# Performance work log

Hardware: AMD Instinct MI355X
Metric: run time of the kernel (lower is better)

The kernel has to match this reference:

```python
import jax, jax.numpy as jnp
import numpy as np
from jax import lax

LIN_DIMS = [(3200, 2048), (2048, 1024), (1024, 512), (512, 256), (256, 128),
            (128, 64), (64, 32), (32, 16), (16, 8), (8, 4), (4, 2), (2, 1)]
BN_EPS = 1e-5


def _conv(x, w, b):
    y = lax.conv_general_dilated(x, w, window_strides=(3, 3),
                                 padding=((1, 1), (1, 1)),
                                 dimension_numbers=('NCHW', 'OIHW', 'NCHW'))
    return y + b.reshape(1, -1, 1, 1)


def _bn(x, g, b):
    # training-mode BatchNorm2d: biased batch statistics over (N, H, W)
    m = jnp.mean(x, axis=(0, 2, 3), keepdims=True)
    v = jnp.var(x, axis=(0, 2, 3), keepdims=True)
    return (x - m) * lax.rsqrt(v + BN_EPS) * g.reshape(1, -1, 1, 1) + b.reshape(1, -1, 1, 1)


def setup_inputs() -> dict:
    key = jax.random.key(0)
    ks = iter(jax.random.split(key, 64))
    d = {}
    d['x'] = jax.random.normal(next(ks), (64, 512, 40, 40), jnp.float32)
    d['conv1_w'] = jax.random.normal(next(ks), (256, 512, 3, 3), jnp.float32) / np.sqrt(512 * 9)
    d['conv1_b'] = jnp.zeros((256,), jnp.float32)
    d['bn1_g'] = jnp.ones((256,), jnp.float32)
    d['bn1_b'] = jnp.zeros((256,), jnp.float32)
    d['conv2_w'] = jax.random.normal(next(ks), (128, 256, 3, 3), jnp.float32) / np.sqrt(256 * 9)
    d['conv2_b'] = jnp.zeros((128,), jnp.float32)
    d['bn2_g'] = jnp.ones((128,), jnp.float32)
    d['bn2_b'] = jnp.zeros((128,), jnp.float32)
    for i, (fin, fout) in enumerate(LIN_DIMS):
        d[f'w{i+3}'] = jax.random.normal(next(ks), (fout, fin), jnp.float32) / np.sqrt(fin)
        d[f'b{i+3}'] = jax.random.normal(next(ks), (fout,), jnp.float32) * 0.01
    return d


def reference(x, conv1_w, conv1_b, bn1_g, bn1_b, conv2_w, conv2_b, bn2_g, bn2_b,
              w3, b3, w4, b4, w5, b5, w6, b6, w7, b7, w8, b8, w9, b9,
              w10, b10, w11, b11, w12, b12, w13, b13, w14, b14):
    h = _bn(_conv(x, conv1_w, conv1_b), bn1_g, bn1_b)          # [B,256,14,14]
    h = _bn(_conv(h, conv2_w, conv2_b), bn2_g, bn2_b)          # [B,128,5,5]
    h = h.reshape(h.shape[0], 3200)
    for w, b in [(w3, b3), (w4, b4), (w5, b5), (w6, b6), (w7, b7), (w8, b8),
                 (w9, b9), (w10, b10), (w11, b11), (w12, b12), (w13, b13), (w14, b14)]:
        h = h @ w.T + b
    return jax.nn.sigmoid(h)                                   # [B,1]
```

## Files before the change

### kernel.cpp

```cpp
#include <hip/hip_runtime.h>
#include <cstdint>
#include <cstddef>

typedef short bf16x8 __attribute__((ext_vector_type(8)));
typedef float f32x4 __attribute__((ext_vector_type(4)));

__device__ __forceinline__ unsigned short f2bf(float f) {
  union { float f; unsigned u; } v; v.f = f;
  unsigned r = v.u + 0x7fffu + ((v.u >> 16) & 1u);
  return (unsigned short)(r >> 16);
}

#define GLOAD_LDS16(gp, lp)                                            \
  __builtin_amdgcn_global_load_lds(                                    \
      (const __attribute__((address_space(1))) void*)(const void*)(gp),\
      (__attribute__((address_space(3))) void*)(void*)(lp), 16, 0, 0)

__global__ __launch_bounds__(256) void cast_bf16(const float* __restrict__ in,
                                                 unsigned short* __restrict__ out, int n4) {
  int i = blockIdx.x * 256 + threadIdx.x;
  if (i < n4) {
    float4 v = ((const float4*)in)[i];
    ushort4 o;
    o.x = f2bf(v.x); o.y = f2bf(v.y); o.z = f2bf(v.z); o.w = f2bf(v.w);
    ((ushort4*)out)[i] = o;
  }
}

__global__ __launch_bounds__(256) void im2col1(const float* __restrict__ x,
                                               unsigned short* __restrict__ A1) {
  __shared__ float buf[64 * 126];
  int t = threadIdx.x;
  int cc = blockIdx.x, oh = blockIdx.y, n = blockIdx.z;
  int ci0 = cc * 64;
  int ih0 = oh * 3 - 1;
  for (int rowid = t; rowid < 192; rowid += 256) {
    int c = rowid / 3, r = rowid - c * 3;
    buf[c * 126 + r * 42 + 0] = 0.f;
    buf[c * 126 + r * 42 + 41] = 0.f;
  }
  for (int idx = t; idx < 1920; idx += 256) {
    int row = idx / 10, ch = idx - row * 10;
    int c = row / 3, r = row - c * 3;
    int ih = ih0 + r;
    float4 v = make_float4(0.f, 0.f, 0.f, 0.f);
    if ((unsigned)ih < 40u)
      v = *(const float4*)(x + (((size_t)n * 512 + ci0 + c) * 40 + ih) * 40 + ch * 4);
    float* dst = buf + c * 126 + r * 42 + 1 + ch * 4;
    dst[0] = v.x; dst[1] = v.y; dst[2] = v.z; dst[3] = v.w;
  }
  __syncthreads();
  for (int idx = t; idx < 2016; idx += 256) {
    int ow = idx / 144, q4 = idx - ow * 144;
    int kk = q4 * 4;
    unsigned short vv[4];
#pragma unroll
    for (int j = 0; j < 4; ++j) {
      int k = kk + j;
      int c = k / 9, rr = k - c * 9;
      int kh = rr / 3, kw = rr - kh * 3;
      vv[j] = f2bf(buf[c * 126 + kh * 42 + 3 * ow + kw]);
    }
    ushort4 o; o.x = vv[0]; o.y = vv[1]; o.z = vv[2]; o.w = vv[3];
    *(ushort4*)(A1 + ((size_t)(n * 196 + oh * 14 + ow)) * 4608 + cc * 576 + kk) = o;
  }
}

__global__ __launch_bounds__(256) void im2col2(const float* __restrict__ C1,
                                               const float* __restrict__ scale,
                                               const float* __restrict__ shift,
                                               unsigned short* __restrict__ A2) {
  unsigned idx = blockIdx.x * 256u + threadIdx.x;
  unsigned m = idx / 2304u;
  unsigned k = idx - m * 2304u;
  unsigned n = m / 25u, sp = m - n * 25u;
  unsigned oh = sp / 5u, ow = sp - oh * 5u;
  int ci = (int)(k / 9u); int r = (int)k - ci * 9;
  int kh = r / 3, kw = r - kh * 3;
  int ih = (int)oh * 3 - 1 + kh, iw = (int)ow * 3 - 1 + kw;
  float v = 0.f;
  if ((unsigned)ih < 14u && (unsigned)iw < 14u)
    v = C1[((size_t)n * 196 + ih * 14 + iw) * 256 + ci] * scale[ci] + shift[ci];
  A2[idx] = f2bf(v);
}

template <int BN>
__global__ __launch_bounds__(256) void gemm_bf16(const unsigned short* __restrict__ A,
                                                 const unsigned short* __restrict__ B,
                                                 float* __restrict__ C,
                                                 int M, int N, int K) {
  __shared__ __align__(16) unsigned short As[64 * 32];
  __shared__ __align__(16) unsigned short Bs[BN * 32];
  constexpr int WN = BN / 2;
  constexpr int NT = WN / 16;
  int m0 = blockIdx.x * 64;
  int n0 = blockIdx.y * BN;
  int t = threadIdx.x;
  int wave = t >> 6, lane = t & 63;
  (void)wave; (void)lane;
  int q = (t & 63) >> 4, mr = t & 15;
  int wm = ((t >> 6) & 1) * 32;
  int wn = (t >> 7) * WN;
  f32x4 acc[2][NT] = {};

  for (int k0 = 0; k0 < K; k0 += 32) {
    __syncthreads();
    GLOAD_LDS16(A + (size_t)(m0 + (t >> 2)) * K + k0 + (t & 3) * 8, As + t * 8);
#pragma unroll
    for (int i = 0; i < BN / 64; ++i) {
      int c = t + i * 256;
      GLOAD_LDS16(B + (size_t)(n0 + (c >> 2)) * K + k0 + (c & 3) * 8, Bs + c * 8);
    }
    __syncthreads();
    bf16x8 af[2];
#pragma unroll
    for (int s = 0; s < 2; ++s)
      af[s] = *((const bf16x8*)(As + (wm + s * 16 + mr) * 32 + q * 8));
#pragma unroll
    for (int nt = 0; nt < NT; ++nt) {
      bf16x8 bfr = *((const bf16x8*)(Bs + (wn + nt * 16 + mr) * 32 + q * 8));
#pragma unroll
      for (int s = 0; s < 2; ++s)
        acc[s][nt] = __builtin_amdgcn_mfma_f32_16x16x32_bf16(af[s], bfr, acc[s][nt], 0, 0, 0);
    }
  }
#pragma unroll
  for (int s = 0; s < 2; ++s)
#pragma unroll
    for (int nt = 0; nt < NT; ++nt)
#pragma unroll
      for (int r = 0; r < 4; ++r)
        C[(size_t)(m0 + wm + s * 16 + q * 4 + r) * N + n0 + wn + nt * 16 + mr] = acc[s][nt][r];
}

__global__ void bn_stats(const float* __restrict__ C, float* __restrict__ sum,
                         float* __restrict__ sumsq, int rowsPerBlock, int ncols) {
  int c = threadIdx.x;
  int r0 = blockIdx.x * rowsPerBlock;
  float s = 0.f, s2 = 0.f;
  for (int r = 0; r < rowsPerBlock; ++r) {
    float v = C[(size_t)(r0 + r) * ncols + c];
    s += v; s2 += v * v;
  }
  atomicAdd(&sum[c], s);
  atomicAdd(&sumsq[c], s2);
}

__global__ void bn_scale(const float* __restrict__ sum, const float* __restrict__ sumsq,
                         const float* __restrict__ g, const float* __restrict__ b,
                         float* __restrict__ scale, float* __restrict__ shift,
                         float inv_count, int nc) {
  int c = blockIdx.x * blockDim.x + threadIdx.x;
  if (c < nc) {
    float m = sum[c] * inv_count;
    float var = sumsq[c] * inv_count - m * m;
    float sc = g[c] / sqrtf(var + 1e-5f);
    scale[c] = sc;
    shift[c] = b[c] - m * sc;
  }
}

__global__ void mlp_head(const float* w14, const float* b14,
                         const float* w13, const float* b13,
                         const float* w12, const float* b12,
                         const float* w11, const float* b11,
                         const float* w10, const float* b10,
                         const float* w9,  const float* b9,
                         const float* w8,  const float* b8,
                         const float* w7,  const float* b7,
                         float* __restrict__ r_out, float* __restrict__ c_out) {
  __shared__ float ra[256], rb[256];
  int t = threadIdx.x;
  float cs = 0.f;
  if (t < 2) ra[t] = w14[t];
  if (t == 0) cs = b14[0];
  __syncthreads();
  const float* Ws[7] = {w13, w12, w11, w10, w9, w8, w7};
  const float* Bs[7] = {b13, b12, b11, b10, b9, b8, b7};
  const int fouts[7] = {2, 4, 8, 16, 32, 64, 128};
  float* cur = ra; float* nxt = rb;
  for (int s = 0; s < 7; ++s) {
    int fo = fouts[s], fi = fo * 2;
    if (t == 0) {
      float d = 0.f;
      for (int i = 0; i < fo; ++i) d += cur[i] * Bs[s][i];
      cs += d;
    }
    if (t < fi) {
      float a = 0.f;
      const float* W = Ws[s];
      for (int i = 0; i < fo; ++i) a += cur[i] * W[i * fi + t];
      nxt[t] = a;
    }
    __syncthreads();
    float* tmp = cur; cur = nxt; nxt = tmp;
  }
  r_out[t] = cur[t];
  if (t == 0) c_out[0] = cs;
}

__global__ void mlp_stage(const float* __restrict__ W, const float* __restrict__ bt,
                          const float* __restrict__ r_in, const float* __restrict__ c_in,
                          float* __restrict__ r_out, float* __restrict__ c_out,
                          int fin, int fout) {
  __shared__ float red[256];
  int t = threadIdx.x;
  int jl = t & 31, ig = t >> 5;
  int j = blockIdx.x * 32 + jl;
  int chunk = fout >> 3;
  int i0 = ig * chunk;
  float acc = 0.f;
  for (int i = i0; i < i0 + chunk; ++i)
    acc += r_in[i] * W[(size_t)i * fin + j];
  red[t] = acc;
  __syncthreads();
  if (ig == 0) {
    float s = 0.f;
#pragma unroll
    for (int u = 0; u < 8; ++u) s += red[u * 32 + jl];
    r_out[j] = s;
  }
  if (blockIdx.x == 0) {
    __syncthreads();
    float p = 0.f;
    for (int i = t; i < fout; i += 256) p += r_in[i] * bt[i];
    red[t] = p;
    __syncthreads();
    for (int s = 128; s > 0; s >>= 1) {
      if (t < s) red[t] += red[t + s];
      __syncthreads();
    }
    if (t == 0) c_out[0] = red[0] + c_in[0];
  }
}

__global__ void final_k(const float* __restrict__ C2, const float* __restrict__ scale2,
                        const float* __restrict__ shift2, const float* __restrict__ r,
                        const float* __restrict__ c_in, float* __restrict__ out) {
  int n = blockIdx.x;
  int t = threadIdx.x;
  float acc = 0.f;
  for (int j = t; j < 3200; j += 256) {
    int c = j / 25, sp = j - c * 25;
    float v = C2[((size_t)n * 25 + sp) * 128 + c] * scale2[c] + shift2[c];
    acc += v * r[j];
  }
  __shared__ float red[256];
  red[t] = acc;
  __syncthreads();
  for (int s = 128; s > 0; s >>= 1) {
    if (t < s) red[t] += red[t + s];
    __syncthreads();
  }
  if (t == 0) {
    float z = red[0] + c_in[0];
    out[n] = 1.f / (1.f + expf(-z));
  }
}

static constexpr size_t OFF_A1   = 0;
static constexpr size_t OFF_W1B  = 115605504;
static constexpr size_t OFF_C1   = 117964800;
static constexpr size_t OFF_A2   = 130809856;
static constexpr size_t OFF_W2B  = 138182656;
static constexpr size_t OFF_C2   = 138772480;
static constexpr size_t OFF_SUM1 = 139591680;
static constexpr size_t OFF_SQ1  = 139592704;
static constexpr size_t OFF_SUM2 = 139593728;
static constexpr size_t OFF_SQ2  = 139594752;
static constexpr size_t OFF_SC1  = 139595776;
static constexpr size_t OFF_SH1  = 139596800;
static constexpr size_t OFF_SC2  = 139597824;
static constexpr size_t OFF_SH2  = 139598848;
static constexpr size_t OFF_RA   = 139599872;
static constexpr size_t OFF_RB   = 139612928;
static constexpr size_t OFF_CA   = 139625984;
static constexpr size_t OFF_CB   = 139626240;

extern "C" void kernel_launch(void* const* d_in, const int* in_sizes, int n_in,
                              void* d_out, int out_size, void* d_ws, size_t ws_size,
                              hipStream_t stream) {
  const float* x   = (const float*)d_in[0];
  const float* w1  = (const float*)d_in[1];
  const float* g1  = (const float*)d_in[3];
  const float* bb1 = (const float*)d_in[4];
  const float* w2  = (const float*)d_in[5];
  const float* g2  = (const float*)d_in[7];
  const float* bb2 = (const float*)d_in[8];

  char* ws = (char*)d_ws;
  unsigned short* A1  = (unsigned short*)(ws + OFF_A1);
  unsigned short* W1b = (unsigned short*)(ws + OFF_W1B);
  float*          C1  = (float*)(ws + OFF_C1);
  unsigned short* A2  = (unsigned short*)(ws + OFF_A2);
  unsigned short* W2b = (unsigned short*)(ws + OFF_W2B);
  float*          C2  = (float*)(ws + OFF_C2);
  float* SUM1 = (float*)(ws + OFF_SUM1);
  float* SQ1  = (float*)(ws + OFF_SQ1);
  float* SUM2 = (float*)(ws + OFF_SUM2);
  float* SQ2  = (float*)(ws + OFF_SQ2);
  float* SC1  = (float*)(ws + OFF_SC1);
  float* SH1  = (float*)(ws + OFF_SH1);
  float* SC2  = (float*)(ws + OFF_SC2);
  float* SH2  = (float*)(ws + OFF_SH2);
  float* RA   = (float*)(ws + OFF_RA);
  float* RB   = (float*)(ws + OFF_RB);
  float* CA   = (float*)(ws + OFF_CA);
  float* CB   = (float*)(ws + OFF_CB);

  hipMemsetAsync(ws + OFF_SUM1, 0, 4096, stream);

  cast_bf16<<<1152, 256, 0, stream>>>(w1, W1b, 294912);
  cast_bf16<<<288, 256, 0, stream>>>(w2, W2b, 73728);

  im2col1<<<dim3(8, 14, 64), 256, 0, stream>>>(x, A1);
  gemm_bf16<128><<<dim3(196, 2), 256, 0, stream>>>(A1, W1b, C1, 12544, 256, 4608);
  bn_stats<<<98, 256, 0, stream>>>(C1, SUM1, SQ1, 128, 256);
  bn_scale<<<1, 256, 0, stream>>>(SUM1, SQ1, g1, bb1, SC1, SH1, 1.f / 12544.f, 256);

  im2col2<<<14400, 256, 0, stream>>>(C1, SC1, SH1, A2);
  gemm_bf16<64><<<dim3(25, 2), 256, 0, stream>>>(A2, W2b, C2, 1600, 128, 2304);
  bn_stats<<<16, 128, 0, stream>>>(C2, SUM2, SQ2, 100, 128);
  bn_scale<<<1, 256, 0, stream>>>(SUM2, SQ2, g2, bb2, SC2, SH2, 1.f / 1600.f, 128);

  mlp_head<<<1, 256, 0, stream>>>(
      (const float*)d_in[31], (const float*)d_in[32],
      (const float*)d_in[29], (const float*)d_in[30],
      (const float*)d_in[27], (const float*)d_in[28],
      (const float*)d_in[25], (const float*)d_in[26],
      (const float*)d_in[23], (const float*)d_in[24],
      (const float*)d_in[21], (const float*)d_in[22],
      (const float*)d_in[19], (const float*)d_in[20],
      (const float*)d_in[17], (const float*)d_in[18],
      RA, CA);
  mlp_stage<<<16, 256, 0, stream>>>((const float*)d_in[15], (const float*)d_in[16],
                                    RA, CA, RB, CB, 512, 256);
  mlp_stage<<<32, 256, 0, stream>>>((const float*)d_in[13], (const float*)d_in[14],
                                    RB, CB, RA, CA, 1024, 512);
  mlp_stage<<<64, 256, 0, stream>>>((const float*)d_in[11], (const float*)d_in[12],
                                    RA, CA, RB, CB, 2048, 1024);
  mlp_stage<<<100, 256, 0, stream>>>((const float*)d_in[9], (const float*)d_in[10],
                                     RB, CB, RA, CA, 3200, 2048);

  final_k<<<64, 256, 0, stream>>>(C2, SC2, SH2, RA, CA, (float*)d_out);
}
```

Measured before the change: 936.2 us.

## Split-K both conv GEMMs with fused partial reduction and BN stats

Adds a blockIdx.z split-K dimension to the bf16 GEMM. Conv1 uses up to 4 K-slices, chosen by available workspace, and conv2 uses 8, to fill more CUs than the 392 and 50 block grids did. Partial sums are combined in a new reduce_stats kernel that also accumulates the BN sum and sum-of-squares. bn_scale is folded into im2col2 and final_k, and the two weight casts are merged into one launch, removing several small launches. The cost is extra global traffic to write and read the partial buffers, plus BN scale being recomputed per element. The workspace layout is reshuffled so C1 reuses A1's region.

```diff
diff --git a/kernel.cpp b/kernel.cpp
--- a/kernel.cpp
+++ b/kernel.cpp
@@ -16,15 +16,19 @@
       (const __attribute__((address_space(1))) void*)(const void*)(gp),\
       (__attribute__((address_space(3))) void*)(void*)(lp), 16, 0, 0)
 
-__global__ __launch_bounds__(256) void cast_bf16(const float* __restrict__ in,
-                                                 unsigned short* __restrict__ out, int n4) {
+__global__ __launch_bounds__(256) void cast2(const float* __restrict__ w1,
+                                             const float* __restrict__ w2,
+                                             unsigned short* __restrict__ W1b,
+                                             unsigned short* __restrict__ W2b) {
   int i = blockIdx.x * 256 + threadIdx.x;
-  if (i < n4) {
-    float4 v = ((const float4*)in)[i];
-    ushort4 o;
-    o.x = f2bf(v.x); o.y = f2bf(v.y); o.z = f2bf(v.z); o.w = f2bf(v.w);
-    ((ushort4*)out)[i] = o;
-  }
+  const float* src; unsigned short* dst; int j;
+  if (i < 294912) { src = w1; dst = W1b; j = i; }
+  else if (i < 368640) { src = w2; dst = W2b; j = i - 294912; }
+  else return;
+  float4 v = ((const float4*)src)[j];
+  ushort4 o;
+  o.x = f2bf(v.x); o.y = f2bf(v.y); o.z = f2bf(v.z); o.w = f2bf(v.w);
+  ((ushort4*)dst)[j] = o;
 }
 
 __global__ __launch_bounds__(256) void im2col1(const float* __restrict__ x,
@@ -67,8 +71,10 @@
 }
 
 __global__ __launch_bounds__(256) void im2col2(const float* __restrict__ C1,
-                                               const float* __restrict__ scale,
-                                               const float* __restrict__ shift,
+                                               const float* __restrict__ SUM1,
+                                               const float* __restrict__ SQ1,
+                                               const float* __restrict__ g,
+                                               const float* __restrict__ b,
                                                unsigned short* __restrict__ A2) {
   unsigned idx = blockIdx.x * 256u + threadIdx.x;
   unsigned m = idx / 2304u;
@@ -79,31 +85,37 @@
   int kh = r / 3, kw = r - kh * 3;
   int ih = (int)oh * 3 - 1 + kh, iw = (int)ow * 3 - 1 + kw;
   float v = 0.f;
-  if ((unsigned)ih < 14u && (unsigned)iw < 14u)
-    v = C1[((size_t)n * 196 + ih * 14 + iw) * 256 + ci] * scale[ci] + shift[ci];
+  if ((unsigned)ih < 14u && (unsigned)iw < 14u) {
+    float mean = SUM1[ci] * (1.f / 12544.f);
+    float var = SQ1[ci] * (1.f / 12544.f) - mean * mean;
+    float sc = g[ci] / sqrtf(var + 1e-5f);
+    float sh = b[ci] - mean * sc;
+    v = C1[((size_t)n * 196 + ih * 14 + iw) * 256 + ci] * sc + sh;
+  }
   A2[idx] = f2bf(v);
 }
 
 template <int BN>
 __global__ __launch_bounds__(256) void gemm_bf16(const unsigned short* __restrict__ A,
                                                  const unsigned short* __restrict__ B,
-                                                 float* __restrict__ C,
-                                                 int M, int N, int K) {
+                                                 float* __restrict__ Cp,
+                                                 int M, int N, int K, int k_chunk) {
   __shared__ __align__(16) unsigned short As[64 * 32];
   __shared__ __align__(16) unsigned short Bs[BN * 32];
   constexpr int WN = BN / 2;
   constexpr int NT = WN / 16;
   int m0 = blockIdx.x * 64;
   int n0 = blockIdx.y * BN;
-  int t = threadIdx.x;
-  int wave = t >> 6, lane = t & 63;
-  (void)wave; (void)lane;
+  int kb = blockIdx.z;
+  Cp += (size_t)kb * M * N;
+  int k_begin = kb * k_chunk;
+  int t = threadIdx.x;
   int q = (t & 63) >> 4, mr = t & 15;
   int wm = ((t >> 6) & 1) * 32;
   int wn = (t >> 7) * WN;
   f32x4 acc[2][NT] = {};
 
-  for (int k0 = 0; k0 < K; k0 += 32) {
+  for (int k0 = k_begin; k0 < k_begin + k_chunk; k0 += 32) {
     __syncthreads();
     GLOAD_LDS16(A + (size_t)(m0 + (t >> 2)) * K + k0 + (t & 3) * 8, As + t * 8);
 #pragma unroll
@@ -130,34 +142,26 @@
     for (int nt = 0; nt < NT; ++nt)
 #pragma unroll
       for (int r = 0; r < 4; ++r)
-        C[(size_t)(m0 + wm + s * 16 + q * 4 + r) * N + n0 + wn + nt * 16 + mr] = acc[s][nt][r];
-}
-
-__global__ void bn_stats(const float* __restrict__ C, float* __restrict__ sum,
-                         float* __restrict__ sumsq, int rowsPerBlock, int ncols) {
+        Cp[(size_t)(m0 + wm + s * 16 + q * 4 + r) * N + n0 + wn + nt * 16 + mr] = acc[s][nt][r];
+}
+
+template <int KS>
+__global__ void reduce_stats(const float* __restrict__ Cp, float* __restrict__ C,
+                             float* __restrict__ sum, float* __restrict__ sumsq,
+                             int rowsPerBlock, int ncols, int MN) {
   int c = threadIdx.x;
   int r0 = blockIdx.x * rowsPerBlock;
   float s = 0.f, s2 = 0.f;
   for (int r = 0; r < rowsPerBlock; ++r) {
-    float v = C[(size_t)(r0 + r) * ncols + c];
+    size_t off = (size_t)(r0 + r) * ncols + c;
+    float v = 0.f;
+#pragma unroll
+    for (int k = 0; k < KS; ++k) v += Cp[(size_t)k * MN + off];
+    C[off] = v;
     s += v; s2 += v * v;
   }
   atomicAdd(&sum[c], s);
   atomicAdd(&sumsq[c], s2);
-}
-
-__global__ void bn_scale(const float* __restrict__ sum, const float* __restrict__ sumsq,
-                         const float* __restrict__ g, const float* __restrict__ b,
-                         float* __restrict__ scale, float* __restrict__ shift,
-                         float inv_count, int nc) {
-  int c = blockIdx.x * blockDim.x + threadIdx.x;
-  if (c < nc) {
-    float m = sum[c] * inv_count;
-    float var = sumsq[c] * inv_count - m * m;
-    float sc = g[c] / sqrtf(var + 1e-5f);
-    scale[c] = sc;
-    shift[c] = b[c] - m * sc;
-  }
 }
 
 __global__ void mlp_head(const float* w14, const float* b14,
@@ -234,15 +238,20 @@
   }
 }
 
-__global__ void final_k(const float* __restrict__ C2, const float* __restrict__ scale2,
-                        const float* __restrict__ shift2, const float* __restrict__ r,
+__global__ void final_k(const float* __restrict__ C2, const float* __restrict__ SUM2,
+                        const float* __restrict__ SQ2, const float* __restrict__ g2,
+                        const float* __restrict__ b2, const float* __restrict__ r,
                         const float* __restrict__ c_in, float* __restrict__ out) {
   int n = blockIdx.x;
   int t = threadIdx.x;
   float acc = 0.f;
   for (int j = t; j < 3200; j += 256) {
     int c = j / 25, sp = j - c * 25;
-    float v = C2[((size_t)n * 25 + sp) * 128 + c] * scale2[c] + shift2[c];
+    float mean = SUM2[c] * (1.f / 1600.f);
+    float var = SQ2[c] * (1.f / 1600.f) - mean * mean;
+    float sc = g2[c] / sqrtf(var + 1e-5f);
+    float sh = b2[c] - mean * sc;
+    float v = C2[((size_t)n * 25 + sp) * 128 + c] * sc + sh;
     acc += v * r[j];
   }
   __shared__ float red[256];
@@ -259,23 +268,18 @@
 }
 
 static constexpr size_t OFF_A1   = 0;
+static constexpr size_t OFF_C1   = 0;
+static constexpr size_t OFF_A2   = 16777216;
+static constexpr size_t OFF_C2P  = 33554432;
+static constexpr size_t OFF_C2   = 41943040;
 static constexpr size_t OFF_W1B  = 115605504;
-static constexpr size_t OFF_C1   = 117964800;
-static constexpr size_t OFF_A2   = 130809856;
-static constexpr size_t OFF_W2B  = 138182656;
-static constexpr size_t OFF_C2   = 138772480;
-static constexpr size_t OFF_SUM1 = 139591680;
-static constexpr size_t OFF_SQ1  = 139592704;
-static constexpr size_t OFF_SUM2 = 139593728;
-static constexpr size_t OFF_SQ2  = 139594752;
-static constexpr size_t OFF_SC1  = 139595776;
-static constexpr size_t OFF_SH1  = 139596800;
-static constexpr size_t OFF_SC2  = 139597824;
-static constexpr size_t OFF_SH2  = 139598848;
-static constexpr size_t OFF_RA   = 139599872;
-static constexpr size_t OFF_RB   = 139612928;
-static constexpr size_t OFF_CA   = 139625984;
-static constexpr size_t OFF_CB   = 139626240;
+static constexpr size_t OFF_W2B  = 117964800;
+static constexpr size_t OFF_STATS= 118554624;
+static constexpr size_t OFF_RA   = 118558720;
+static constexpr size_t OFF_RB   = 118571776;
+static constexpr size_t OFF_CA   = 118584832;
+static constexpr size_t OFF_CB   = 118584960;
+static constexpr size_t OFF_C1P  = 118585344;
 
 extern "C" void kernel_launch(void* const* d_in, const int* in_sizes, int n_in,
                               void* d_out, int out_size, void* d_ws, size_t ws_size,
@@ -290,38 +294,43 @@
 
   char* ws = (char*)d_ws;
   unsigned short* A1  = (unsigned short*)(ws + OFF_A1);
-  unsigned short* W1b = (unsigned short*)(ws + OFF_W1B);
   float*          C1  = (float*)(ws + OFF_C1);
   unsigned short* A2  = (unsigned short*)(ws + OFF_A2);
+  float*          C2P = (float*)(ws + OFF_C2P);
+  float*          C2  = (float*)(ws + OFF_C2);
+  unsigned short* W1b = (unsigned short*)(ws + OFF_W1B);
   unsigned short* W2b = (unsigned short*)(ws + OFF_W2B);
-  float*          C2  = (float*)(ws + OFF_C2);
-  float* SUM1 = (float*)(ws + OFF_SUM1);
-  float* SQ1  = (float*)(ws + OFF_SQ1);
-  float* SUM2 = (float*)(ws + OFF_SUM2);
-  float* SQ2  = (float*)(ws + OFF_SQ2);
-  float* SC1  = (float*)(ws + OFF_SC1);
-  float* SH1  = (float*)(ws + OFF_SH1);
-  float* SC2  = (float*)(ws + OFF_SC2);
-  float* SH2  = (float*)(ws + OFF_SH2);
+  float* SUM1 = (float*)(ws + OFF_STATS);
+  float* SQ1  = (float*)(ws + OFF_STATS + 1024);
+  float* SUM2 = (float*)(ws + OFF_STATS + 2048);
+  float* SQ2  = (float*)(ws + OFF_STATS + 3072);
   float* RA   = (float*)(ws + OFF_RA);
   float* RB   = (float*)(ws + OFF_RB);
   float* CA   = (float*)(ws + OFF_CA);
   float* CB   = (float*)(ws + OFF_CB);
-
-  hipMemsetAsync(ws + OFF_SUM1, 0, 4096, stream);
-
-  cast_bf16<<<1152, 256, 0, stream>>>(w1, W1b, 294912);
-  cast_bf16<<<288, 256, 0, stream>>>(w2, W2b, 73728);
+  float* C1P  = (float*)(ws + OFF_C1P);
+
+  const size_t cpart = 12845056;
+  int ks1 = (ws_size >= OFF_C1P + 4 * cpart) ? 4
+          : (ws_size >= OFF_C1P + 2 * cpart) ? 2 : 1;
+
+  hipMemsetAsync(ws + OFF_STATS, 0, 4096, stream);
+
+  cast2<<<1440, 256, 0, stream>>>(w1, w2, W1b, W2b);
 
   im2col1<<<dim3(8, 14, 64), 256, 0, stream>>>(x, A1);
-  gemm_bf16<128><<<dim3(196, 2), 256, 0, stream>>>(A1, W1b, C1, 12544, 256, 4608);
-  bn_stats<<<98, 256, 0, stream>>>(C1, SUM1, SQ1, 128, 256);
-  bn_scale<<<1, 256, 0, stream>>>(SUM1, SQ1, g1, bb1, SC1, SH1, 1.f / 12544.f, 256);
-
-  im2col2<<<14400, 256, 0, stream>>>(C1, SC1, SH1, A2);
-  gemm_bf16<64><<<dim3(25, 2), 256, 0, stream>>>(A2, W2b, C2, 1600, 128, 2304);
-  bn_stats<<<16, 128, 0, stream>>>(C2, SUM2, SQ2, 100, 128);
-  bn_scale<<<1, 256, 0, stream>>>(SUM2, SQ2, g2, bb2, SC2, SH2, 1.f / 1600.f, 128);
+  gemm_bf16<128><<<dim3(196, 2, ks1), 256, 0, stream>>>(A1, W1b, C1P, 12544, 256, 4608,
+                                                        4608 / ks1);
+  if (ks1 == 4)
+    reduce_stats<4><<<392, 256, 0, stream>>>(C1P, C1, SUM1, SQ1, 32, 256, 3211264);
+  else if (ks1 == 2)
+    reduce_stats<2><<<392, 256, 0, stream>>>(C1P, C1, SUM1, SQ1, 32, 256, 3211264);
+  else
+    reduce_stats<1><<<392, 256, 0, stream>>>(C1P, C1, SUM1, SQ1, 32, 256, 3211264);
+
+  im2col2<<<14400, 256, 0, stream>>>(C1, SUM1, SQ1, g1, bb1, A2);
+  gemm_bf16<64><<<dim3(25, 2, 8), 256, 0, stream>>>(A2, W2b, C2P, 1600, 128, 2304, 288);
+  reduce_stats<8><<<100, 128, 0, stream>>>(C2P, C2, SUM2, SQ2, 16, 128, 204800);
 
   mlp_head<<<1, 256, 0, stream>>>(
       (const float*)d_in[31], (const float*)d_in[32],
@@ -342,5 +351,5 @@
   mlp_stage<<<100, 256, 0, stream>>>((const float*)d_in[9], (const float*)d_in[10],
                                      RB, CB, RA, CA, 3200, 2048);
 
-  final_k<<<64, 256, 0, stream>>>(C2, SC2, SH2, RA, CA, (float*)d_out);
-}
+  final_k<<<64, 256, 0, stream>>>(C2, SUM2, SQ2, g2, bb2, RA, CA, (float*)d_out);
+}
```

After: 849.1 us. -9.3%, faster.
